# Performance work log

Measured on AMD Instinct MI355X. Metric: run time of the kernel, lower is better.

Reference implementation:

```python
import jax, jax.numpy as jnp
import numpy as np

NUM_LAYER = 5
EMB = 300
N_NODES = 100000
N_EDGES = 250000
BN_EPS = 1e-5


def setup_inputs() -> dict:
    key = jax.random.key(0)
    ks = jax.random.split(key, 12)
    s = 0.05
    inp = {
        "x": jax.random.randint(ks[0], (N_NODES, 2), 0, 3),
        "edge_index": jax.random.randint(ks[1], (2, N_EDGES), 0, N_NODES),
        "edge_attr": jax.random.randint(ks[2], (N_EDGES, 2), 0, 3),
        # node-feature embedding tables
        "x_emb1": jax.random.normal(ks[3], (120, EMB), jnp.float32) * s,
        "x_emb2": jax.random.normal(ks[4], (3, EMB), jnp.float32) * s,
        # per-layer edge embedding tables (bond type=6, bond direction=3)
        "e_emb1": jax.random.normal(ks[5], (NUM_LAYER, 6, EMB), jnp.float32) * s,
        "e_emb2": jax.random.normal(ks[6], (NUM_LAYER, 3, EMB), jnp.float32) * s,
        # per-layer GIN MLP: Linear(D,2D) -> ReLU -> Linear(2D,D); weights stored (out,in)
        "w1": jax.random.normal(ks[7], (NUM_LAYER, 2 * EMB, EMB), jnp.float32) * s,
        "b1": jnp.zeros((NUM_LAYER, 2 * EMB), jnp.float32),
        "w2": jax.random.normal(ks[8], (NUM_LAYER, EMB, 2 * EMB), jnp.float32) * s,
        "b2": jnp.zeros((NUM_LAYER, EMB), jnp.float32),
        # per-layer BatchNorm1d affine params (training-mode batch stats)
        "gamma": jnp.ones((NUM_LAYER, EMB), jnp.float32),
        "beta": jnp.zeros((NUM_LAYER, EMB), jnp.float32),
    }
    return inp


def reference(x, edge_index, edge_attr, x_emb1, x_emb2, e_emb1, e_emb2, w1, b1, w2, b2, gamma, beta):
    n = x.shape[0]
    # input node embedding: atom type + chirality tag
    h = x_emb1[x[:, 0]] + x_emb2[x[:, 1]]  # [N, D]

    # add self loops (self-loop edge_attr = [4, 0])
    loop = jnp.arange(n, dtype=edge_index.dtype)
    src = jnp.concatenate([edge_index[0], loop])  # [E+N]
    dst = jnp.concatenate([edge_index[1], loop])
    ea0 = jnp.concatenate([edge_attr[:, 0], jnp.full((n,), 4, edge_attr.dtype)])
    ea1 = jnp.concatenate([edge_attr[:, 1], jnp.zeros((n,), edge_attr.dtype)])

    for l in range(NUM_LAYER):
        e = e_emb1[l][ea0] + e_emb2[l][ea1]           # [E+N, D] edge embeddings
        msg = h[src] + e                               # gather + message
        agg = jax.ops.segment_sum(msg, dst, num_segments=n)  # scatter-add aggregate
        hid = jnp.maximum(agg @ w1[l].T + b1[l], 0.0)  # GIN MLP
        h2 = hid @ w2[l].T + b2[l]
        # BatchNorm1d (training-mode batch statistics, biased variance)
        mu = h2.mean(axis=0)
        var = jnp.mean((h2 - mu) ** 2, axis=0)
        h2 = (h2 - mu) * jax.lax.rsqrt(var + BN_EPS) * gamma[l] + beta[l]
        if l < NUM_LAYER - 1:
            h2 = jnp.maximum(h2, 0.0)  # ReLU (dropout ratio = 0)
        h = h2

    # JK == 'last'
    return h
```

## Files before the change

kernel.cpp:

```cpp
#include <hip/hip_runtime.h>
#include <hip/hip_bf16.h>

#define DD 300
#define C4 75
#define BN_EPS 1e-5f

typedef _Float16 f16x8 __attribute__((ext_vector_type(8)));
typedef float f32x4 __attribute__((ext_vector_type(4)));

union PackH4 { _Float16 h[4]; uint2 u; };

__device__ __forceinline__ void gld_lds16(const void* g, void* lds) {
    __builtin_amdgcn_global_load_lds(
        (const __attribute__((address_space(1))) void*)g,
        (__attribute__((address_space(3))) void*)lds, 16, 0, 0);
}

__global__ __launch_bounds__(256) void embed_kernel(
    const int* __restrict__ x, const float* __restrict__ emb1,
    const float* __restrict__ emb2, float* __restrict__ h, int total4)
{
    int i = blockIdx.x * 256 + threadIdx.x;
    if (i >= total4) return;
    int node = i / C4, chunk = i - node * C4;
    int a = x[2 * node], b = x[2 * node + 1];
    int c = chunk << 2;
    float4 v1 = *(const float4*)(emb1 + (size_t)a * DD + c);
    float4 v2 = *(const float4*)(emb2 + (size_t)b * DD + c);
    float4 r;
    r.x = v1.x + v2.x; r.y = v1.y + v2.y; r.z = v1.z + v2.z; r.w = v1.w + v2.w;
    *(float4*)(h + (size_t)node * DD + c) = r;
}

__global__ __launch_bounds__(256) void build_ec_kernel(
    const float* __restrict__ e1, const float* __restrict__ e2, float* __restrict__ ec)
{
    int gid = blockIdx.x * 256 + threadIdx.x;
    if (gid >= 5 * 18 * DD) return;
    int l = gid / (18 * DD);
    int rem = gid - l * 18 * DD;
    int combo = rem / DD;
    int c = rem - combo * DD;
    int a0 = combo / 3, a1 = combo - a0 * 3;
    ec[gid] = e1[(size_t)l * 6 * DD + a0 * DD + c] + e2[(size_t)l * 3 * DD + a1 * DD + c];
}

__global__ __launch_bounds__(256) void deg_kernel(
    const int* __restrict__ ei, int* __restrict__ deg, int E)
{
    int e = blockIdx.x * 256 + threadIdx.x;
    if (e >= E) return;
    atomicAdd(&deg[ei[E + e]], 1);
}

__global__ __launch_bounds__(256) void scan1_kernel(
    const int* __restrict__ deg, int* __restrict__ pre, int* __restrict__ blockSum, int n)
{
    __shared__ int sa[256], sb[256];
    int t = threadIdx.x;
    int base = blockIdx.x * 1024 + t * 4;
    int v0 = (base + 0 < n) ? deg[base + 0] : 0;
    int v1 = (base + 1 < n) ? deg[base + 1] : 0;
    int v2 = (base + 2 < n) ? deg[base + 2] : 0;
    int v3 = (base + 3 < n) ? deg[base + 3] : 0;
    int tot = v0 + v1 + v2 + v3;
    sa[t] = tot;
    __syncthreads();
    int* src = sa; int* dst = sb;
    for (int off = 1; off < 256; off <<= 1) {
        int v = src[t];
        if (t >= off) v += src[t - off];
        dst[t] = v;
        __syncthreads();
        int* tmp = src; src = dst; dst = tmp;
    }
    int incl = src[t];
    int excl = incl - tot;
    if (base + 0 < n) pre[base + 0] = excl;
    if (base + 1 < n) pre[base + 1] = excl + v0;
    if (base + 2 < n) pre[base + 2] = excl + v0 + v1;
    if (base + 3 < n) pre[base + 3] = excl + v0 + v1 + v2;
    if (t == 255) blockSum[blockIdx.x] = incl;
}

__global__ __launch_bounds__(256) void scan2_kernel(int* __restrict__ blockSum, int nb)
{
    __shared__ int sa[256], sb[256];
    int t = threadIdx.x;
    int v = (t < nb) ? blockSum[t] : 0;
    sa[t] = v;
    __syncthreads();
    int* src = sa; int* dst = sb;
    for (int off = 1; off < 256; off <<= 1) {
        int x = src[t];
        if (t >= off) x += src[t - off];
        dst[t] = x;
        __syncthreads();
        int* tmp = src; src = dst; dst = tmp;
    }
    if (t < nb) blockSum[t] = src[t] - v;
}

__global__ __launch_bounds__(256) void scan3_kernel(
    const int* __restrict__ pre, const int* __restrict__ blockSum,
    int* __restrict__ rowPtr, int* __restrict__ cursor, int n, int E)
{
    int idx = blockIdx.x * 256 + threadIdx.x;
    if (idx > n) return;
    int v = (idx < n) ? pre[idx] + blockSum[idx >> 10] : E;
    rowPtr[idx] = v;
    if (idx < n) cursor[idx] = v;
}

__global__ __launch_bounds__(256) void fill_kernel(
    const int* __restrict__ ei, const int* __restrict__ ea,
    int* __restrict__ cursor, int* __restrict__ edges, int E)
{
    int e = blockIdx.x * 256 + threadIdx.x;
    if (e >= E) return;
    int src = ei[e];
    int dst = ei[E + e];
    int combo = ea[2 * e] * 3 + ea[2 * e + 1];
    int slot = atomicAdd(&cursor[dst], 1);
    edges[slot] = src | (combo << 18);
}

__global__ __launch_bounds__(256) void gather_kernel(
    const float* __restrict__ h, const int* __restrict__ rowPtr,
    const int* __restrict__ edges, const float* __restrict__ ec,
    const float* __restrict__ scale, const float* __restrict__ shift, int use_affine,
    _Float16* __restrict__ agg, int n)
{
    int gid = blockIdx.x * 256 + threadIdx.x;
    int node = gid / C4, ch = gid - node * C4;
    if (node >= n) return;
    int c = ch << 2;
    float4 sc, sh;
    if (use_affine) {
        sc = *(const float4*)(scale + c);
        sh = *(const float4*)(shift + c);
    }
    float4 acc = *(const float4*)(h + (size_t)node * DD + c);
    if (use_affine) {
        acc.x = fmaxf(fmaf(sc.x, acc.x, sh.x), 0.f);
        acc.y = fmaxf(fmaf(sc.y, acc.y, sh.y), 0.f);
        acc.z = fmaxf(fmaf(sc.z, acc.z, sh.z), 0.f);
        acc.w = fmaxf(fmaf(sc.w, acc.w, sh.w), 0.f);
    }
    float4 es = *(const float4*)(ec + 12 * DD + c);
    acc.x += es.x; acc.y += es.y; acc.z += es.z; acc.w += es.w;

    int start = rowPtr[node], end = rowPtr[node + 1];
    for (int e = start; e < end; ++e) {
        int pk = edges[e];
        int src = pk & 0x3FFFF;
        int combo = pk >> 18;
        float4 hv = *(const float4*)(h + (size_t)src * DD + c);
        if (use_affine) {
            hv.x = fmaxf(fmaf(sc.x, hv.x, sh.x), 0.f);
            hv.y = fmaxf(fmaf(sc.y, hv.y, sh.y), 0.f);
            hv.z = fmaxf(fmaf(sc.z, hv.z, sh.z), 0.f);
            hv.w = fmaxf(fmaf(sc.w, hv.w, sh.w), 0.f);
        }
        float4 ev = *(const float4*)(ec + combo * DD + c);
        acc.x += hv.x + ev.x;
        acc.y += hv.y + ev.y;
        acc.z += hv.z + ev.z;
        acc.w += hv.w + ev.w;
    }
    PackH4 p;
    p.h[0] = (_Float16)acc.x;
    p.h[1] = (_Float16)acc.y;
    p.h[2] = (_Float16)acc.z;
    p.h[3] = (_Float16)acc.w;
    *(uint2*)(agg + (size_t)node * 320 + c) = p.u;
}

__global__ __launch_bounds__(256) void convert_w_kernel(
    const float* __restrict__ w, _Float16* __restrict__ wf,
    int rows, int cols, int rowsP, int colsP)
{
    int gid = blockIdx.x * 256 + threadIdx.x;
    int total = 5 * rowsP * colsP;
    if (gid >= total) return;
    int l = gid / (rowsP * colsP);
    int rem = gid - l * (rowsP * colsP);
    int r = rem / colsP;
    int k = rem - r * colsP;
    float v = (r < rows && k < cols) ? w[((size_t)l * rows + r) * cols + k] : 0.f;
    wf[gid] = (_Float16)v;
}

template <bool OUT_F16, bool DO_STATS>
__global__ __launch_bounds__(256) void mfma_gemm_lds(
    const _Float16* __restrict__ A, const _Float16* __restrict__ W,
    const float* __restrict__ bias,
    _Float16* __restrict__ outH, float* __restrict__ outF,
    float* __restrict__ sum, float* __restrict__ sumsq,
    int M, int Kp, int outStride, int outN, int nCol)
{
    __shared__ __attribute__((aligned(16))) unsigned short sA[128 * 64];
    __shared__ __attribute__((aligned(16))) unsigned short sB[128 * 64];

    const int bid = blockIdx.x;
    const int group = bid / (8 * nCol);
    const int within = bid - group * 8 * nCol;
    const int rowT = group * 8 + (within & 7);
    const int colT = within >> 3;
    const int bm = rowT << 7;
    const int bn = colT << 7;

    const int tid = threadIdx.x;
    const int lane = tid & 63, wv = tid >> 6;
    const int wy = wv & 1, wx = wv >> 1;
    const int quad = lane >> 4, l16 = lane & 15;

    const int r8 = lane >> 3;
    const int chv = (lane & 7) ^ r8;

    f32x4 acc[4][4] = {};

    for (int k0 = 0; k0 < Kp; k0 += 64) {
        __syncthreads();
#pragma unroll
        for (int j = 0; j < 4; ++j) {
            int rloc = wv * 32 + j * 8 + r8;
            int ldsBase = (wv * 32 + j * 8) * 64;
            gld_lds16(A + (size_t)(bm + rloc) * Kp + k0 + chv * 8, &sA[ldsBase]);
            gld_lds16(W + (size_t)(bn + rloc) * Kp + k0 + chv * 8, &sB[ldsBase]);
        }
        __syncthreads();
#pragma unroll
        for (int kk = 0; kk < 2; ++kk) {
            f16x8 a[4], b[4];
#pragma unroll
            for (int i = 0; i < 4; ++i) {
                int rA = wy * 64 + i * 16 + l16;
                int slotA = (kk * 4 + quad) ^ (rA & 7);
                a[i] = *(const f16x8*)&sA[rA * 64 + slotA * 8];
                int rB = wx * 64 + i * 16 + l16;
                int slotB = (kk * 4 + quad) ^ (rB & 7);
                b[i] = *(const f16x8*)&sB[rB * 64 + slotB * 8];
            }
#pragma unroll
            for (int i = 0; i < 4; ++i)
#pragma unroll
                for (int j = 0; j < 4; ++j)
                    acc[i][j] = __builtin_amdgcn_mfma_f32_16x16x32_f16(
                        a[i], b[j], acc[i][j], 0, 0, 0);
        }
    }

#pragma unroll
    for (int j = 0; j < 4; ++j) {
        int col = bn + wx * 64 + j * 16 + l16;
        float bv = (col < outN) ? bias[col] : 0.f;
        float cs = 0.f, cq = 0.f;
#pragma unroll
        for (int i = 0; i < 4; ++i) {
            int rowBase = bm + wy * 64 + i * 16 + (quad << 2);
#pragma unroll
            for (int r = 0; r < 4; ++r) {
                int row = rowBase + r;
                if (row >= M) continue;
                float v = acc[i][j][r] + bv;
                if constexpr (DO_STATS) { cs += v; cq += v * v; }
                if constexpr (OUT_F16) {
                    float o = (col < outN) ? fmaxf(v, 0.f) : 0.f;
                    outH[(size_t)row * outStride + col] = (_Float16)o;
                } else {
                    if (col < outN) outF[(size_t)row * outStride + col] = v;
                }
            }
        }
        if constexpr (DO_STATS) {
            cs += __shfl_down(cs, 32); cq += __shfl_down(cq, 32);
            cs += __shfl_down(cs, 16); cq += __shfl_down(cq, 16);
            if (quad == 0 && col < outN) {
                atomicAdd(&sum[col], cs);
                atomicAdd(&sumsq[col], cq);
            }
        }
    }
}

__global__ void finalize_kernel(
    const float* __restrict__ sum, const float* __restrict__ sumsq,
    const float* __restrict__ gamma, const float* __restrict__ beta,
    float* __restrict__ scale, float* __restrict__ shift, float inv_n)
{
    int c = threadIdx.x;
    if (c < DD) {
        float mu = sum[c] * inv_n;
        float var = sumsq[c] * inv_n - mu * mu;
        float inv = rsqrtf(var + BN_EPS);
        float sc = gamma[c] * inv;
        scale[c] = sc;
        shift[c] = fmaf(-mu, sc, beta[c]);
    }
}

__global__ __launch_bounds__(256) void apply_kernel(
    const float* __restrict__ h, const float* __restrict__ scale,
    const float* __restrict__ shift, float* __restrict__ out, int total4)
{
    int i = blockIdx.x * 256 + threadIdx.x;
    if (i >= total4) return;
    int c = (i % C4) << 2;
    float4 v = ((const float4*)h)[i];
    float4 r;
    r.x = fmaf(scale[c + 0], v.x, shift[c + 0]);
    r.y = fmaf(scale[c + 1], v.y, shift[c + 1]);
    r.z = fmaf(scale[c + 2], v.z, shift[c + 2]);
    r.w = fmaf(scale[c + 3], v.w, shift[c + 3]);
    ((float4*)out)[i] = r;
}

extern "C" void kernel_launch(void* const* d_in, const int* in_sizes, int n_in,
                              void* d_out, int out_size, void* d_ws, size_t ws_size,
                              hipStream_t stream)
{
    const int*   x      = (const int*)d_in[0];
    const int*   ei     = (const int*)d_in[1];
    const int*   ea     = (const int*)d_in[2];
    const float* x_emb1 = (const float*)d_in[3];
    const float* x_emb2 = (const float*)d_in[4];
    const float* e_emb1 = (const float*)d_in[5];
    const float* e_emb2 = (const float*)d_in[6];
    const float* w1     = (const float*)d_in[7];
    const float* b1     = (const float*)d_in[8];
    const float* w2     = (const float*)d_in[9];
    const float* b2     = (const float*)d_in[10];
    const float* gamma  = (const float*)d_in[11];
    const float* beta   = (const float*)d_in[12];

    const int n = in_sizes[0] / 2;
    const int E = in_sizes[1] / 2;
    const int nRowT = (n + 127) / 128;
    const int nRowTP = ((nRowT + 7) / 8) * 8;
    const int MpA = nRowTP * 128;
    const int Kp1 = 320, Kp2 = 640;
    const int NP1 = 640, NP2 = 384;

    char* p = (char*)d_ws;
    auto alloc = [&](size_t bytes) -> void* {
        void* r = (void*)p;
        p += (bytes + 255) & ~(size_t)255;
        return r;
    };
    _Float16* agg  = (_Float16*)alloc((size_t)MpA * Kp1 * 2);
    _Float16* hid  = (_Float16*)alloc((size_t)MpA * Kp2 * 2);
    _Float16* w1f  = (_Float16*)alloc((size_t)5 * NP1 * Kp1 * 2);
    _Float16* w2f  = (_Float16*)alloc((size_t)5 * NP2 * Kp2 * 2);
    float* ec     = (float*)alloc((size_t)5 * 18 * DD * 4);
    int*   deg    = (int*)alloc((size_t)n * 4);
    int*   rowPtr = (int*)alloc((size_t)(n + 1) * 4);
    int*   cursor = (int*)alloc((size_t)n * 4);
    int*   blockSum = (int*)alloc(256 * 4);
    int*   edges  = (int*)alloc((size_t)E * 4);
    float* sum   = (float*)alloc(320 * 4);
    float* sumsq = (float*)alloc(320 * 4);
    float* scale = (float*)alloc(320 * 4);
    float* shift = (float*)alloc(320 * 4);

    float* h = (float*)d_out;
    const int total4 = n * C4;
    const int nb = (n + 1023) / 1024;

    {
        convert_w_kernel<<<(5 * NP1 * Kp1 + 255) / 256, 256, 0, stream>>>(w1, w1f, 600, 300, NP1, Kp1);
        convert_w_kernel<<<(5 * NP2 * Kp2 + 255) / 256, 256, 0, stream>>>(w2, w2f, 300, 600, NP2, Kp2);
        build_ec_kernel<<<(5 * 18 * DD + 255) / 256, 256, 0, stream>>>(e_emb1, e_emb2, ec);
        hipMemsetAsync(deg, 0, (size_t)n * 4, stream);
        deg_kernel<<<(E + 255) / 256, 256, 0, stream>>>(ei, deg, E);
        scan1_kernel<<<nb, 256, 0, stream>>>(deg, cursor , blockSum, n);
        scan2_kernel<<<1, 256, 0, stream>>>(blockSum, nb);
        scan3_kernel<<<(n + 256) / 256, 256, 0, stream>>>(cursor, blockSum, rowPtr, deg , n, E);
        fill_kernel<<<(E + 255) / 256, 256, 0, stream>>>(ei, ea, deg, edges, E);
        hipMemsetAsync(agg, 0, (size_t)MpA * Kp1 * 2, stream);
        embed_kernel<<<(total4 + 255) / 256, 256, 0, stream>>>(x, x_emb1, x_emb2, h, total4);
    }

    const int gatherTotal = n * C4;
    const int nCol1 = NP1 / 128;
    const int nCol2 = NP2 / 128;
    const int g1 = nRowTP * nCol1;
    const int g2 = nRowTP * nCol2;

    for (int l = 0; l < 5; l++) {
        hipMemsetAsync(sum, 0, 2 * 320 * sizeof(float), stream);
        gather_kernel<<<(gatherTotal + 255) / 256, 256, 0, stream>>>(
            h, rowPtr, edges, ec + (size_t)l * 18 * DD, scale, shift, l > 0 ? 1 : 0,
            agg, n);
        mfma_gemm_lds<true, false><<<g1, 256, 0, stream>>>(
            agg, w1f + (size_t)l * NP1 * Kp1,
            b1 + (size_t)l * 600, hid, nullptr, nullptr, nullptr,
            n, Kp1, Kp2, 600, nCol1);
        mfma_gemm_lds<false, true><<<g2, 256, 0, stream>>>(
            hid, w2f + (size_t)l * NP2 * Kp2,
            b2 + (size_t)l * 300, nullptr, h, sum, sumsq,
            n, Kp2, 300, 300, nCol2);
        finalize_kernel<<<1, 320, 0, stream>>>(sum, sumsq, gamma + (size_t)l * DD,
                                               beta + (size_t)l * DD, scale, shift,
                                               1.0f / (float)n);
    }
    apply_kernel<<<(total4 + 255) / 256, 256, 0, stream>>>(h, scale, shift, h, total4);
}
```

Measured before the change: 1.935 ms.

## Double-buffer GEMM LDS tiles and pad intermediate h rows to 320

```diff
diff --git a/kernel.cpp b/kernel.cpp
--- a/kernel.cpp
+++ b/kernel.cpp
@@ -18,7 +18,7 @@
 
 __global__ __launch_bounds__(256) void embed_kernel(
     const int* __restrict__ x, const float* __restrict__ emb1,
-    const float* __restrict__ emb2, float* __restrict__ h, int total4)
+    const float* __restrict__ emb2, float* __restrict__ h, int hs, int total4)
 {
     int i = blockIdx.x * 256 + threadIdx.x;
     if (i >= total4) return;
@@ -29,7 +29,7 @@
     float4 v2 = *(const float4*)(emb2 + (size_t)b * DD + c);
     float4 r;
     r.x = v1.x + v2.x; r.y = v1.y + v2.y; r.z = v1.z + v2.z; r.w = v1.w + v2.w;
-    *(float4*)(h + (size_t)node * DD + c) = r;
+    *(float4*)(h + (size_t)node * hs + c) = r;
 }
 
 __global__ __launch_bounds__(256) void build_ec_kernel(
@@ -126,7 +126,7 @@
 }
 
 __global__ __launch_bounds__(256) void gather_kernel(
-    const float* __restrict__ h, const int* __restrict__ rowPtr,
+    const float* __restrict__ h, int hs, const int* __restrict__ rowPtr,
     const int* __restrict__ edges, const float* __restrict__ ec,
     const float* __restrict__ scale, const float* __restrict__ shift, int use_affine,
     _Float16* __restrict__ agg, int n)
@@ -140,7 +140,7 @@
         sc = *(const float4*)(scale + c);
         sh = *(const float4*)(shift + c);
     }
-    float4 acc = *(const float4*)(h + (size_t)node * DD + c);
+    float4 acc = *(const float4*)(h + (size_t)node * hs + c);
     if (use_affine) {
         acc.x = fmaxf(fmaf(sc.x, acc.x, sh.x), 0.f);
         acc.y = fmaxf(fmaf(sc.y, acc.y, sh.y), 0.f);
@@ -155,7 +155,7 @@
         int pk = edges[e];
         int src = pk & 0x3FFFF;
         int combo = pk >> 18;
-        float4 hv = *(const float4*)(h + (size_t)src * DD + c);
+        float4 hv = *(const float4*)(h + (size_t)src * hs + c);
         if (use_affine) {
             hv.x = fmaxf(fmaf(sc.x, hv.x, sh.x), 0.f);
             hv.y = fmaxf(fmaf(sc.y, hv.y, sh.y), 0.f);
@@ -199,8 +199,8 @@
     float* __restrict__ sum, float* __restrict__ sumsq,
     int M, int Kp, int outStride, int outN, int nCol)
 {
-    __shared__ __attribute__((aligned(16))) unsigned short sA[128 * 64];
-    __shared__ __attribute__((aligned(16))) unsigned short sB[128 * 64];
+    __shared__ __attribute__((aligned(16))) unsigned short sA[2][128 * 64];
+    __shared__ __attribute__((aligned(16))) unsigned short sB[2][128 * 64];
 
     const int bid = blockIdx.x;
     const int group = bid / (8 * nCol);
@@ -220,16 +220,17 @@
 
     f32x4 acc[4][4] = {};
 
-    for (int k0 = 0; k0 < Kp; k0 += 64) {
-        __syncthreads();
+    auto stage = [&](int buf, int k0) {
 #pragma unroll
         for (int j = 0; j < 4; ++j) {
             int rloc = wv * 32 + j * 8 + r8;
             int ldsBase = (wv * 32 + j * 8) * 64;
-            gld_lds16(A + (size_t)(bm + rloc) * Kp + k0 + chv * 8, &sA[ldsBase]);
-            gld_lds16(W + (size_t)(bn + rloc) * Kp + k0 + chv * 8, &sB[ldsBase]);
+            gld_lds16(A + (size_t)(bm + rloc) * Kp + k0 + chv * 8, &sA[buf][ldsBase]);
+            gld_lds16(W + (size_t)(bn + rloc) * Kp + k0 + chv * 8, &sB[buf][ldsBase]);
         }
-        __syncthreads();
+    };
+
+    auto compute = [&](int buf) {
 #pragma unroll
         for (int kk = 0; kk < 2; ++kk) {
             f16x8 a[4], b[4];
@@ -237,10 +238,10 @@
             for (int i = 0; i < 4; ++i) {
                 int rA = wy * 64 + i * 16 + l16;
                 int slotA = (kk * 4 + quad) ^ (rA & 7);
-                a[i] = *(const f16x8*)&sA[rA * 64 + slotA * 8];
+                a[i] = *(const f16x8*)&sA[buf][rA * 64 + slotA * 8];
                 int rB = wx * 64 + i * 16 + l16;
                 int slotB = (kk * 4 + quad) ^ (rB & 7);
-                b[i] = *(const f16x8*)&sB[rB * 64 + slotB * 8];
+                b[i] = *(const f16x8*)&sB[buf][rB * 64 + slotB * 8];
             }
 #pragma unroll
             for (int i = 0; i < 4; ++i)
@@ -249,7 +250,19 @@
                     acc[i][j] = __builtin_amdgcn_mfma_f32_16x16x32_f16(
                         a[i], b[j], acc[i][j], 0, 0, 0);
         }
-    }
+    };
+
+    const int nT = Kp >> 6;
+    stage(0, 0);
+    __syncthreads();
+    int cur = 0;
+    for (int t = 0; t < nT - 1; ++t) {
+        stage(cur ^ 1, (t + 1) << 6);
+        compute(cur);
+        __syncthreads();
+        cur ^= 1;
+    }
+    compute(cur);
 
 #pragma unroll
     for (int j = 0; j < 4; ++j) {
@@ -264,12 +277,12 @@
                 int row = rowBase + r;
                 if (row >= M) continue;
                 float v = acc[i][j][r] + bv;
-                if constexpr (DO_STATS) { cs += v; cq += v * v; }
+                if constexpr (DO_STATS) { if (col < outN) { cs += v; cq += v * v; } }
                 if constexpr (OUT_F16) {
                     float o = (col < outN) ? fmaxf(v, 0.f) : 0.f;
                     outH[(size_t)row * outStride + col] = (_Float16)o;
                 } else {
-                    if (col < outN) outF[(size_t)row * outStride + col] = v;
+                    if (col < outStride) outF[(size_t)row * outStride + col] = v;
                 }
             }
         }
@@ -301,13 +314,14 @@
 }
 
 __global__ __launch_bounds__(256) void apply_kernel(
-    const float* __restrict__ h, const float* __restrict__ scale,
+    const float* __restrict__ h, int hs, const float* __restrict__ scale,
     const float* __restrict__ shift, float* __restrict__ out, int total4)
 {
     int i = blockIdx.x * 256 + threadIdx.x;
     if (i >= total4) return;
-    int c = (i % C4) << 2;
-    float4 v = ((const float4*)h)[i];
+    int node = i / C4;
+    int c = (i - node * C4) << 2;
+    float4 v = *(const float4*)(h + (size_t)node * hs + c);
     float4 r;
     r.x = fmaf(scale[c + 0], v.x, shift[c + 0]);
     r.y = fmaf(scale[c + 1], v.y, shift[c + 1]);
@@ -363,7 +377,18 @@
     float* scale = (float*)alloc(320 * 4);
     float* shift = (float*)alloc(320 * 4);
 
-    float* h = (float*)d_out;
+    const size_t used = (size_t)(p - (char*)d_ws);
+    const size_t hBytes = (size_t)n * 320 * 4;
+    float* h;
+    int HS;
+    if (ws_size >= used + hBytes) {
+        h = (float*)alloc(hBytes);
+        HS = 320;
+    } else {
+        h = (float*)d_out;
+        HS = DD;
+    }
+
     const int total4 = n * C4;
     const int nb = (n + 1023) / 1024;
 
@@ -378,7 +403,7 @@
         scan3_kernel<<<(n + 256) / 256, 256, 0, stream>>>(cursor, blockSum, rowPtr, deg , n, E);
         fill_kernel<<<(E + 255) / 256, 256, 0, stream>>>(ei, ea, deg, edges, E);
         hipMemsetAsync(agg, 0, (size_t)MpA * Kp1 * 2, stream);
-        embed_kernel<<<(total4 + 255) / 256, 256, 0, stream>>>(x, x_emb1, x_emb2, h, total4);
+        embed_kernel<<<(total4 + 255) / 256, 256, 0, stream>>>(x, x_emb1, x_emb2, h, HS, total4);
     }
 
     const int gatherTotal = n * C4;
@@ -390,7 +415,7 @@
     for (int l = 0; l < 5; l++) {
         hipMemsetAsync(sum, 0, 2 * 320 * sizeof(float), stream);
         gather_kernel<<<(gatherTotal + 255) / 256, 256, 0, stream>>>(
-            h, rowPtr, edges, ec + (size_t)l * 18 * DD, scale, shift, l > 0 ? 1 : 0,
+            h, HS, rowPtr, edges, ec + (size_t)l * 18 * DD, scale, shift, l > 0 ? 1 : 0,
             agg, n);
         mfma_gemm_lds<true, false><<<g1, 256, 0, stream>>>(
             agg, w1f + (size_t)l * NP1 * Kp1,
@@ -399,10 +424,11 @@
         mfma_gemm_lds<false, true><<<g2, 256, 0, stream>>>(
             hid, w2f + (size_t)l * NP2 * Kp2,
             b2 + (size_t)l * 300, nullptr, h, sum, sumsq,
-            n, Kp2, 300, 300, nCol2);
+            n, Kp2, HS, 300, nCol2);
         finalize_kernel<<<1, 320, 0, stream>>>(sum, sumsq, gamma + (size_t)l * DD,
                                                beta + (size_t)l * DD, scale, shift,
                                                1.0f / (float)n);
     }
-    apply_kernel<<<(total4 + 255) / 256, 256, 0, stream>>>(h, scale, shift, h, total4);
-}
+    apply_kernel<<<(total4 + 255) / 256, 256, 0, stream>>>(h, HS, scale, shift,
+                                                           (float*)d_out, total4);
+}
```

New measurement: 2.197 ms. +13.5%, slower.
